# Optimization experiments

Hardware: AMD Instinct MI355X
Metric: run time of the kernel (lower is better)

Reference implementation:

```python
import jax, jax.numpy as jnp
import numpy as np

N_NODES = 50000
N_EDGES = 400000
DIM = 128
NUM_ANCHORS = 32
NEG_SLOPE = 0.01  # torch F.leaky_relu default


def setup_inputs() -> dict:
    key = jax.random.key(0)
    k1, k2, k3, k4 = jax.random.split(key, 4)
    x = jax.random.normal(k1, (N_NODES, DIM), dtype=jnp.float32)
    edge_index = jax.random.randint(k2, (2, N_EDGES), 0, N_NODES, dtype=jnp.int64)
    # Linear(2*dim, num_anchors): W [out, in], bias [out] (zeros here)
    W = jax.random.normal(k3, (NUM_ANCHORS, 2 * DIM), dtype=jnp.float32) * 0.05
    b_lin = jnp.zeros((NUM_ANCHORS,), dtype=jnp.float32)
    # glorot-style anchor prompt [num_anchors, dim]
    anchor = jax.random.normal(k4, (NUM_ANCHORS, DIM), dtype=jnp.float32) * 0.1
    return {"x": x, "edge_index": edge_index, "layer": 0,
            "W": W, "b_lin": b_lin, "anchor": anchor}


def reference(x, edge_index, layer, W, b_lin, anchor):
    # layer is the index into the (single-layer) parameter lists; params passed directly.
    del layer
    src = x[edge_index[0]]               # [E, dim] gather
    dst = x[edge_index[1]]               # [E, dim] gather
    combined = jnp.concatenate([src, dst], axis=1)          # [E, 2*dim]
    logits = combined @ W.T + b_lin                         # [E, num_anchors]
    logits = jnp.where(logits >= 0, logits, NEG_SLOPE * logits)  # leaky_relu
    b = jax.nn.softmax(logits, axis=1)                      # [E, num_anchors]
    prompt = b @ anchor                                     # [E, dim]
    return prompt
```

## Files before the change

### kernel.cpp

```cpp
#include <hip/hip_runtime.h>

#define N_NODES 50000
#define N_EDGES 400000
#define DIM 128
#define NA 32
#define NEG 0.01f

__global__ __launch_bounds__(256) void proj_kernel(const float* __restrict__ x,
                                                   const float* __restrict__ W,
                                                   float* __restrict__ proj) {
    __shared__ float Wl[64 * 128];
    const int t = threadIdx.x;
    for (int i = 0; i < 32; ++i) {
        int idx = i * 256 + t;
        int a = idx >> 7, k = idx & 127;
        Wl[idx] = (a < 32) ? W[a * 256 + k] : W[(a - 32) * 256 + 128 + k];
    }
    __syncthreads();

    const int n0 = blockIdx.x * 128 + (t & 63);
    const int n1 = n0 + 64;
    const int w = t >> 6;
    const int n0c = n0 < N_NODES ? n0 : 0;
    const int n1c = n1 < N_NODES ? n1 : 0;

    const float4* x4 = (const float4*)x;
    float acc0[16], acc1[16];
#pragma unroll
    for (int i = 0; i < 16; ++i) { acc0[i] = 0.f; acc1[i] = 0.f; }

#pragma unroll 1
    for (int kc = 0; kc < 32; ++kc) {
        float4 xv0 = x4[n0c * 32 + kc];
        float4 xv1 = x4[n1c * 32 + kc];
        const float* wbase = &Wl[(w * 16) * 128 + kc * 4];
#pragma unroll
        for (int i = 0; i < 16; ++i) {
            float4 wv = *(const float4*)(wbase + i * 128);
            acc0[i] += xv0.x * wv.x; acc1[i] += xv1.x * wv.x;
            acc0[i] += xv0.y * wv.y; acc1[i] += xv1.y * wv.y;
            acc0[i] += xv0.z * wv.z; acc1[i] += xv1.z * wv.z;
            acc0[i] += xv0.w * wv.w; acc1[i] += xv1.w * wv.w;
        }
    }

    float4* p4 = (float4*)proj;
    if (n0 < N_NODES) {
#pragma unroll
        for (int j = 0; j < 4; ++j)
            p4[n0 * 16 + w * 4 + j] =
                make_float4(acc0[4 * j], acc0[4 * j + 1], acc0[4 * j + 2], acc0[4 * j + 3]);
    }
    if (n1 < N_NODES) {
#pragma unroll
        for (int j = 0; j < 4; ++j)
            p4[n1 * 16 + w * 4 + j] =
                make_float4(acc1[4 * j], acc1[4 * j + 1], acc1[4 * j + 2], acc1[4 * j + 3]);
    }
}

__global__ __launch_bounds__(256) void edge_kernel(const float* __restrict__ proj,
                                                   const int* __restrict__ ei,
                                                   const float* __restrict__ b_lin,
                                                   const float* __restrict__ anchor,
                                                   float* __restrict__ out,
                                                   int nwaves_total) {
    __shared__ float4 anc4[NA * 32];
    __shared__ float bl[4 * 64];

    const int t = threadIdx.x;
    {
        const float4* a4 = (const float4*)anchor;
        for (int i = t; i < NA * 32; i += 256) anc4[i] = a4[i];
    }
    __syncthreads();

    const int l = t & 63;
    const int wv = t >> 6;
    const int a = l & 31;
    const int hh = l >> 5;
    const float bias = b_lin[a];
    const int wgid = blockIdx.x * 4 + wv;
    const int NP = N_EDGES / 2;

    for (int p = wgid; p < NP; p += nwaves_total) {
        const int e = 2 * p + hh;
        const int s = ei[e];
        const int d = ei[N_EDGES + e];
        float lg = proj[s * 64 + a] + proj[d * 64 + 32 + a] + bias;
        lg = lg >= 0.f ? lg : NEG * lg;

        float m = lg;
#pragma unroll
        for (int off = 16; off; off >>= 1) m = fmaxf(m, __shfl_xor(m, off, 64));
        float pe = __expf(lg - m);
        float sm = pe;
#pragma unroll
        for (int off = 16; off; off >>= 1) sm += __shfl_xor(sm, off, 64);
        float bv = pe / sm;

        bl[wv * 64 + l] = bv;
        asm volatile("s_waitcnt lgkmcnt(0)" ::: "memory");

        float4 acc = make_float4(0.f, 0.f, 0.f, 0.f);
        const float4* blq = (const float4*)&bl[wv * 64 + hh * 32];
#pragma unroll
        for (int q = 0; q < 8; ++q) {
            float4 bq = blq[q];
#pragma unroll
            for (int j = 0; j < 4; ++j) {
                const float bs = (j == 0) ? bq.x : (j == 1) ? bq.y : (j == 2) ? bq.z : bq.w;
                float4 an = anc4[(q * 4 + j) * 32 + a];
                acc.x += bs * an.x;
                acc.y += bs * an.y;
                acc.z += bs * an.z;
                acc.w += bs * an.w;
            }
        }
        ((float4*)out)[e * 32 + a] = acc;
        asm volatile("" ::: "memory");
    }
}

extern "C" void kernel_launch(void* const* d_in, const int* in_sizes, int n_in,
                              void* d_out, int out_size, void* d_ws, size_t ws_size,
                              hipStream_t stream) {
    const float* x = (const float*)d_in[0];
    const int* ei = (const int*)d_in[1];
    const float* W = (const float*)d_in[3];
    const float* b_lin = (const float*)d_in[4];
    const float* anchor = (const float*)d_in[5];
    float* out = (float*)d_out;
    float* proj = (float*)d_ws;

    proj_kernel<<<(N_NODES + 127) / 128, 256, 0, stream>>>(x, W, proj);

    const int blocksB = 2048;
    edge_kernel<<<blocksB, 256, 0, stream>>>(proj, ei, b_lin, anchor, out, blocksB * 4);
}
```

Measured before the change: 311.2 us.

## Software-pipeline edge index and proj gathers, keep anchors in registers

The edge loop now prefetches edge indices two iterations ahead and proj values one iteration ahead, so the dependent gather latency overlaps the softmax and anchor matvec. The anchor matrix moves from LDS into 128 registers per thread, and launch bounds are set to two blocks per CU. The softmax division becomes a hardware reciprocal multiply. In exchange, register pressure rises sharply, which may cap occupancy or cause spills, and the reciprocal is slightly less accurate.

Result: slower. 323.3 us (+3.9%).

```diff
diff --git a/kernel.cpp b/kernel.cpp
--- a/kernel.cpp
+++ b/kernel.cpp
@@ -59,35 +59,48 @@
     }
 }
 
-__global__ __launch_bounds__(256) void edge_kernel(const float* __restrict__ proj,
-                                                   const int* __restrict__ ei,
-                                                   const float* __restrict__ b_lin,
-                                                   const float* __restrict__ anchor,
-                                                   float* __restrict__ out,
-                                                   int nwaves_total) {
-    __shared__ float4 anc4[NA * 32];
+__global__ __launch_bounds__(256, 2) void edge_kernel(const float* __restrict__ proj,
+                                                      const int* __restrict__ ei,
+                                                      const float* __restrict__ b_lin,
+                                                      const float* __restrict__ anchor,
+                                                      float* __restrict__ out,
+                                                      int nwaves_total) {
     __shared__ float bl[4 * 64];
 
     const int t = threadIdx.x;
-    {
-        const float4* a4 = (const float4*)anchor;
-        for (int i = t; i < NA * 32; i += 256) anc4[i] = a4[i];
-    }
-    __syncthreads();
-
     const int l = t & 63;
     const int wv = t >> 6;
     const int a = l & 31;
     const int hh = l >> 5;
+
+    float4 anc[32];
+    {
+        const float4* a4 = (const float4*)anchor;
+#pragma unroll
+        for (int q = 0; q < 32; ++q) anc[q] = a4[q * 32 + a];
+    }
     const float bias = b_lin[a];
-    const int wgid = blockIdx.x * 4 + wv;
+
+    const int S = nwaves_total;
     const int NP = N_EDGES / 2;
+    int p = blockIdx.x * 4 + wv;
 
-    for (int p = wgid; p < NP; p += nwaves_total) {
-        const int e = 2 * p + hh;
-        const int s = ei[e];
-        const int d = ei[N_EDGES + e];
-        float lg = proj[s * 64 + a] + proj[d * 64 + 32 + a] + bias;
+    int s0 = 0, d0 = 0, s1 = 0, d1 = 0;
+    if (p < NP)      { s0 = ei[2 * p + hh];        d0 = ei[N_EDGES + 2 * p + hh]; }
+    if (p + S < NP)  { s1 = ei[2 * (p + S) + hh];  d1 = ei[N_EDGES + 2 * (p + S) + hh]; }
+    float ps = proj[s0 * 64 + a];
+    float pd = proj[d0 * 64 + 32 + a];
+
+    for (; p < NP; p += S) {
+        int s2 = 0, d2 = 0;
+        if (p + 2 * S < NP) {
+            s2 = ei[2 * (p + 2 * S) + hh];
+            d2 = ei[N_EDGES + 2 * (p + 2 * S) + hh];
+        }
+        float psn = proj[s1 * 64 + a];
+        float pdn = proj[d1 * 64 + 32 + a];
+
+        float lg = ps + pd + bias;
         lg = lg >= 0.f ? lg : NEG * lg;
 
         float m = lg;
@@ -97,7 +110,7 @@
         float sm = pe;
 #pragma unroll
         for (int off = 16; off; off >>= 1) sm += __shfl_xor(sm, off, 64);
-        float bv = pe / sm;
+        float bv = pe * __builtin_amdgcn_rcpf(sm);
 
         bl[wv * 64 + l] = bv;
         asm volatile("s_waitcnt lgkmcnt(0)" ::: "memory");
@@ -105,20 +118,23 @@
         float4 acc = make_float4(0.f, 0.f, 0.f, 0.f);
         const float4* blq = (const float4*)&bl[wv * 64 + hh * 32];
 #pragma unroll
-        for (int q = 0; q < 8; ++q) {
-            float4 bq = blq[q];
+        for (int q8 = 0; q8 < 8; ++q8) {
+            float4 bq = blq[q8];
 #pragma unroll
             for (int j = 0; j < 4; ++j) {
                 const float bs = (j == 0) ? bq.x : (j == 1) ? bq.y : (j == 2) ? bq.z : bq.w;
-                float4 an = anc4[(q * 4 + j) * 32 + a];
+                float4 an = anc[q8 * 4 + j];
                 acc.x += bs * an.x;
                 acc.y += bs * an.y;
                 acc.z += bs * an.z;
                 acc.w += bs * an.w;
             }
         }
+        const int e = 2 * p + hh;
         ((float4*)out)[e * 32 + a] = acc;
-        asm volatile("" ::: "memory");
+
+        s1 = s2; d1 = d2;
+        ps = psn; pd = pdn;
     }
 }
 
```

## Fuse projection and edge kernels into one cooperative kernel with grid sync

Applied to the files above, without the earlier changes.

Merges the per-node projection and the per-edge softmax/anchor mix into a single cooperative launch of 1024 blocks, separated by a grid-wide barrier. This removes one kernel launch and the gap between the two kernels. The projection is recomputed in two halves so W fits in the shared buffer that is later reused for the anchors. The softmax drops the max subtraction and uses DPP row reductions plus a fast reciprocal instead of shuffle trees and a divide. Skipping the max step risks overflow for large logits. The grid sync and the halved projection tiling (each x row is read twice) add their own cost.

Result: slower. 630.7 us (+102.7%).

```diff
diff --git a/kernel.cpp b/kernel.cpp
--- a/kernel.cpp
+++ b/kernel.cpp
@@ -1,124 +1,129 @@
 #include <hip/hip_runtime.h>
+#include <hip/hip_cooperative_groups.h>
+
+namespace cg = cooperative_groups;
 
 #define N_NODES 50000
 #define N_EDGES 400000
-#define DIM 128
 #define NA 32
 #define NEG 0.01f
+#define GRID_N 1024
 
-__global__ __launch_bounds__(256) void proj_kernel(const float* __restrict__ x,
-                                                   const float* __restrict__ W,
-                                                   float* __restrict__ proj) {
-    __shared__ float Wl[64 * 128];
-    const int t = threadIdx.x;
-    for (int i = 0; i < 32; ++i) {
-        int idx = i * 256 + t;
-        int a = idx >> 7, k = idx & 127;
-        Wl[idx] = (a < 32) ? W[a * 256 + k] : W[(a - 32) * 256 + 128 + k];
-    }
-    __syncthreads();
+#define DPP_ADD(v, ctrl, rmask)                                                            \
+    v += __int_as_float(__builtin_amdgcn_update_dpp(0, __float_as_int(v), ctrl, rmask, 0xf, true))
 
-    const int n0 = blockIdx.x * 128 + (t & 63);
-    const int n1 = n0 + 64;
-    const int w = t >> 6;
-    const int n0c = n0 < N_NODES ? n0 : 0;
-    const int n1c = n1 < N_NODES ? n1 : 0;
-
-    const float4* x4 = (const float4*)x;
-    float acc0[16], acc1[16];
-#pragma unroll
-    for (int i = 0; i < 16; ++i) { acc0[i] = 0.f; acc1[i] = 0.f; }
-
-#pragma unroll 1
-    for (int kc = 0; kc < 32; ++kc) {
-        float4 xv0 = x4[n0c * 32 + kc];
-        float4 xv1 = x4[n1c * 32 + kc];
-        const float* wbase = &Wl[(w * 16) * 128 + kc * 4];
-#pragma unroll
-        for (int i = 0; i < 16; ++i) {
-            float4 wv = *(const float4*)(wbase + i * 128);
-            acc0[i] += xv0.x * wv.x; acc1[i] += xv1.x * wv.x;
-            acc0[i] += xv0.y * wv.y; acc1[i] += xv1.y * wv.y;
-            acc0[i] += xv0.z * wv.z; acc1[i] += xv1.z * wv.z;
-            acc0[i] += xv0.w * wv.w; acc1[i] += xv1.w * wv.w;
-        }
-    }
-
-    float4* p4 = (float4*)proj;
-    if (n0 < N_NODES) {
-#pragma unroll
-        for (int j = 0; j < 4; ++j)
-            p4[n0 * 16 + w * 4 + j] =
-                make_float4(acc0[4 * j], acc0[4 * j + 1], acc0[4 * j + 2], acc0[4 * j + 3]);
-    }
-    if (n1 < N_NODES) {
-#pragma unroll
-        for (int j = 0; j < 4; ++j)
-            p4[n1 * 16 + w * 4 + j] =
-                make_float4(acc1[4 * j], acc1[4 * j + 1], acc1[4 * j + 2], acc1[4 * j + 3]);
-    }
-}
-
-__global__ __launch_bounds__(256) void edge_kernel(const float* __restrict__ proj,
-                                                   const int* __restrict__ ei,
-                                                   const float* __restrict__ b_lin,
-                                                   const float* __restrict__ anchor,
-                                                   float* __restrict__ out,
-                                                   int nwaves_total) {
-    __shared__ float4 anc4[NA * 32];
+__global__ __launch_bounds__(256, 4) void fused_kernel(
+        const float* __restrict__ x, const int* __restrict__ ei,
+        const float* __restrict__ W, const float* __restrict__ b_lin,
+        const float* __restrict__ anchor, float* __restrict__ proj,
+        float* __restrict__ out) {
+    __shared__ float Sh[4096];
     __shared__ float bl[4 * 64];
 
     const int t = threadIdx.x;
-    {
-        const float4* a4 = (const float4*)anchor;
-        for (int i = t; i < NA * 32; i += 256) anc4[i] = a4[i];
-    }
-    __syncthreads();
-
     const int l = t & 63;
     const int wv = t >> 6;
     const int a = l & 31;
     const int hh = l >> 5;
+
+    const float4* x4 = (const float4*)x;
+    for (int h = 0; h < 2; ++h) {
+        __syncthreads();
+        for (int i = t; i < 4096; i += 256) {
+            int r = i >> 7, k = i & 127;
+            Sh[i] = W[r * 256 + h * 128 + k];
+        }
+        __syncthreads();
+        for (int chunk = blockIdx.x; chunk * 64 < N_NODES; chunk += gridDim.x) {
+            int n = chunk * 64 + l;
+            int nc = n < N_NODES ? n : N_NODES - 1;
+            float acc[8];
+#pragma unroll
+            for (int i = 0; i < 8; ++i) acc[i] = 0.f;
+#pragma unroll 1
+            for (int kc = 0; kc < 32; ++kc) {
+                float4 xv = x4[nc * 32 + kc];
+                const float* wb = &Sh[(wv * 8) * 128 + kc * 4];
+#pragma unroll
+                for (int i = 0; i < 8; ++i) {
+                    float4 wr = *(const float4*)(wb + i * 128);
+                    acc[i] += xv.x * wr.x; acc[i] += xv.y * wr.y;
+                    acc[i] += xv.z * wr.z; acc[i] += xv.w * wr.w;
+                }
+            }
+            if (n < N_NODES) {
+                float4* p4 = (float4*)proj;
+#pragma unroll
+                for (int j = 0; j < 2; ++j)
+                    p4[n * 16 + h * 8 + wv * 2 + j] = make_float4(
+                        acc[4 * j], acc[4 * j + 1], acc[4 * j + 2], acc[4 * j + 3]);
+            }
+        }
+    }
+
+    __threadfence();
+    cg::this_grid().sync();
+    __threadfence();
+
+    {
+        const float4* a4 = (const float4*)anchor;
+        float4* s4 = (float4*)Sh;
+        for (int i = t; i < 1024; i += 256) s4[i] = a4[i];
+    }
+    __syncthreads();
+
     const float bias = b_lin[a];
-    const int wgid = blockIdx.x * 4 + wv;
+    const float4* anc4 = (const float4*)Sh;
     const int NP = N_EDGES / 2;
+    const int S = GRID_N * 4;
 
-    for (int p = wgid; p < NP; p += nwaves_total) {
+    for (int p = blockIdx.x * 4 + wv; p < NP; p += S) {
         const int e = 2 * p + hh;
         const int s = ei[e];
         const int d = ei[N_EDGES + e];
         float lg = proj[s * 64 + a] + proj[d * 64 + 32 + a] + bias;
         lg = lg >= 0.f ? lg : NEG * lg;
+        float pe = __expf(lg);
 
-        float m = lg;
-#pragma unroll
-        for (int off = 16; off; off >>= 1) m = fmaxf(m, __shfl_xor(m, off, 64));
-        float pe = __expf(lg - m);
-        float sm = pe;
-#pragma unroll
-        for (int off = 16; off; off >>= 1) sm += __shfl_xor(sm, off, 64);
-        float bv = pe / sm;
+        float r = pe;
+        DPP_ADD(r, 0x111, 0xf);
+        DPP_ADD(r, 0x112, 0xf);
+        DPP_ADD(r, 0x114, 0xf);
+        DPP_ADD(r, 0x118, 0xf);
+        DPP_ADD(r, 0x142, 0xa);
+        float sm = __shfl(r, 31, 32);
+        float bv = pe * __builtin_amdgcn_rcpf(sm);
 
         bl[wv * 64 + l] = bv;
         asm volatile("s_waitcnt lgkmcnt(0)" ::: "memory");
 
-        float4 acc = make_float4(0.f, 0.f, 0.f, 0.f);
+        float4 acc = {0.f, 0.f, 0.f, 0.f};
         const float4* blq = (const float4*)&bl[wv * 64 + hh * 32];
 #pragma unroll
-        for (int q = 0; q < 8; ++q) {
-            float4 bq = blq[q];
-#pragma unroll
-            for (int j = 0; j < 4; ++j) {
-                const float bs = (j == 0) ? bq.x : (j == 1) ? bq.y : (j == 2) ? bq.z : bq.w;
-                float4 an = anc4[(q * 4 + j) * 32 + a];
-                acc.x += bs * an.x;
-                acc.y += bs * an.y;
-                acc.z += bs * an.z;
-                acc.w += bs * an.w;
+        for (int j = 0; j < 8; ++j) {
+            float4 b4 = blq[j];
+            {
+                float4 an = anc4[(4 * j + 0) * 32 + a];
+                acc.x += b4.x * an.x; acc.y += b4.x * an.y;
+                acc.z += b4.x * an.z; acc.w += b4.x * an.w;
+            }
+            {
+                float4 an = anc4[(4 * j + 1) * 32 + a];
+                acc.x += b4.y * an.x; acc.y += b4.y * an.y;
+                acc.z += b4.y * an.z; acc.w += b4.y * an.w;
+            }
+            {
+                float4 an = anc4[(4 * j + 2) * 32 + a];
+                acc.x += b4.z * an.x; acc.y += b4.z * an.y;
+                acc.z += b4.z * an.z; acc.w += b4.z * an.w;
+            }
+            {
+                float4 an = anc4[(4 * j + 3) * 32 + a];
+                acc.x += b4.w * an.x; acc.y += b4.w * an.y;
+                acc.z += b4.w * an.z; acc.w += b4.w * an.w;
             }
         }
         ((float4*)out)[e * 32 + a] = acc;
-        asm volatile("" ::: "memory");
     }
 }
 
@@ -133,8 +138,8 @@
     float* out = (float*)d_out;
     float* proj = (float*)d_ws;
 
-    proj_kernel<<<(N_NODES + 127) / 128, 256, 0, stream>>>(x, W, proj);
-
-    const int blocksB = 2048;
-    edge_kernel<<<blocksB, 256, 0, stream>>>(proj, ei, b_lin, anchor, out, blocksB * 4);
+    void* args[] = {(void*)&x, (void*)&ei, (void*)&W, (void*)&b_lin,
+                    (void*)&anchor, (void*)&proj, (void*)&out};
+    hipLaunchCooperativeKernel((const void*)fused_kernel, dim3(GRID_N), dim3(256),
+                               args, 0, stream);
 }
```
